# Performance work log

Hardware: AMD Instinct MI355X
Metric: run time of the kernel (lower is better)

Reference implementation:

```python
import jax, jax.numpy as jnp
import numpy as np

B, T, DIM, FF, E, TOPK = 2, 2048, 1024, 4096, 8, 2


def setup_inputs() -> dict:
    key = jax.random.key(0)
    k0, k1, k2, k3 = jax.random.split(key, 4)
    x = jax.random.normal(k0, (B, T, DIM), jnp.float32)
    # router weight [E, D] (nn.Linear(dim, num_experts, bias=False))
    Wr = jax.random.normal(k1, (E, DIM), jnp.float32) * (DIM ** -0.5)
    # per-expert FFN weights, stacked: W1 [E, D, FF], W2 [E, FF, D]
    W1 = jax.random.normal(k2, (E, DIM, FF), jnp.float32) * (DIM ** -0.5)
    W2 = jax.random.normal(k3, (E, FF, DIM), jnp.float32) * (FF ** -0.5)
    return {"x": x, "Wr": Wr, "W1": W1, "W2": W2}


def reference(x, Wr, W1, W2):
    """MoEFeedForward.forward, world_size=1, STANDARD implementation.

    Math: per token, top_k experts by router logits, softmax over the top_k
    logits (fp32), y = sum_k w_k * FFN_{e_k}(x). The torch code realizes this
    via sort/permute + per-expert variable-size GEMM + weighted index_add;
    the scatter-add result is identical to the dense masked form below,
    which is the jit-friendly (static-shape) expression.
    """
    Bn, Tn, D = x.shape
    num_experts = Wr.shape[0]
    xf = x.reshape(-1, D)                      # [N, D], N = B*T
    N = xf.shape[0]

    logits = xf @ Wr.T                         # [N, E]
    topw, topi = jax.lax.top_k(logits, TOPK)   # [N, K]
    topw = jax.nn.softmax(topw.astype(jnp.float32), axis=-1).astype(x.dtype)

    # combine weight for each (token, expert): [N, E] (0 if not routed)
    combine = jnp.zeros((N, num_experts), x.dtype)
    combine = combine.at[jnp.arange(N)[:, None], topi].add(topw)

    out = jnp.zeros_like(xf)
    for e in range(num_experts):               # fixed small loop over experts
        h = jax.nn.gelu(xf @ W1[e], approximate=False)  # exact GELU (nn.GELU)
        out = out + combine[:, e:e + 1] * (h @ W2[e])
    return out.reshape(Bn, Tn, D)
```

## Files before the change

kernel.cpp:

```cpp
#include <hip/hip_runtime.h>
#include <hip/hip_bf16.h>
#include <hip/hip_fp16.h>

#define NTOK 4096
#define DIM 1024
#define FF 4096
#define NE 8
#define NSLOT 8192

typedef _Float16 half8 __attribute__((ext_vector_type(8)));
typedef _Float16 half4 __attribute__((ext_vector_type(4)));
typedef float floatx4 __attribute__((ext_vector_type(4)));

__device__ __forceinline__ float gelu_exact(float x) {
    return 0.5f * x * (1.0f + erff(x * 0.70710678118654752f));
}

__device__ __forceinline__ void gl_lds16(const void* g, void* l) {
    __builtin_amdgcn_global_load_lds(
        (const __attribute__((address_space(1))) void*)g,
        (__attribute__((address_space(3))) void*)l, 16, 0, 0);
}

__device__ __forceinline__ void transpose_tile128(const float* __restrict__ s,
                                                  _Float16* __restrict__ d,
                                                  int R, int C, int r0, int c0,
                                                  char* smem) {
    float (*t)[66] = (float (*)[66])smem;
    int tid = threadIdx.x;
    int rr = tid >> 4, cc = (tid & 15) * 4;
#pragma unroll
    for (int i = 0; i < 8; ++i) {
        float4 v = *(const float4*)(s + (size_t)(r0 + rr + i * 16) * C + c0 + cc);
        t[rr + i * 16][cc] = v.x; t[rr + i * 16][cc + 1] = v.y;
        t[rr + i * 16][cc + 2] = v.z; t[rr + i * 16][cc + 3] = v.w;
    }
    __syncthreads();
#pragma unroll
    for (int j = 0; j < 4; ++j) {
        int chunk = j * 256 + tid;
        int fr = chunk >> 4, ch = chunk & 15;
        half8 v;
#pragma unroll
        for (int u = 0; u < 8; ++u) v[u] = (_Float16)t[ch * 8 + u][fr];
        *(half8*)(d + (size_t)(c0 + fr) * R + r0 + ch * 8) = v;
    }
}

__global__ __launch_bounds__(256) void k_prep(
    const float* __restrict__ x,
    const float* __restrict__ Wr,
    const float* __restrict__ W1,
    _Float16* __restrict__ w1t,
    _Float16* __restrict__ xh,
    int* __restrict__ counts,
    int* __restrict__ tok_e,
    float* __restrict__ tok_w,
    int* __restrict__ tok_pos) {
    __shared__ char smem[33792];
    int bid = blockIdx.x;
    int q = bid / 7, r = bid % 7;
    int tid = threadIdx.x;
    if (r < 4) {
        int t = q * 4 + r;
        int e = t >> 9, rem = t & 511;
        int r0 = (rem >> 6) << 7, c0 = (rem & 63) << 6;
        transpose_tile128(W1 + (size_t)e * DIM * FF, w1t + (size_t)e * FF * DIM,
                          DIM, FF, r0, c0, smem);
    } else if (r < 6) {
        int i = (q * 2 + (r - 4)) * 2048 + tid * 8;
        float4 a = *(const float4*)(x + i);
        float4 b = *(const float4*)(x + i + 4);
        half8 h;
        h[0] = (_Float16)a.x; h[1] = (_Float16)a.y; h[2] = (_Float16)a.z; h[3] = (_Float16)a.w;
        h[4] = (_Float16)b.x; h[5] = (_Float16)b.y; h[6] = (_Float16)b.z; h[7] = (_Float16)b.w;
        *(half8*)(xh + i) = h;
    } else {
        float* wr = (float*)smem;
        for (int i = tid; i < NE * DIM / 4; i += 256)
            ((float4*)wr)[i] = ((const float4*)Wr)[i];
        __syncthreads();
        int w = tid >> 6, lane = tid & 63;
        int t = q * 4 + w;
        float acc[NE] = {};
        for (int j = 0; j < DIM / 64; ++j) {
            float xv = x[t * DIM + j * 64 + lane];
#pragma unroll
            for (int e = 0; e < NE; ++e)
                acc[e] += xv * wr[e * DIM + j * 64 + lane];
        }
#pragma unroll
        for (int e = 0; e < NE; ++e) {
#pragma unroll
            for (int s = 32; s; s >>= 1) acc[e] += __shfl_xor(acc[e], s, 64);
        }
        if (lane == 0) {
            int b0 = 0; float m0 = acc[0];
#pragma unroll
            for (int e = 1; e < NE; ++e) { if (acc[e] > m0) { m0 = acc[e]; b0 = e; } }
            int b1 = -1; float m1 = -1e30f;
#pragma unroll
            for (int e = 0; e < NE; ++e) { if (e != b0 && acc[e] > m1) { m1 = acc[e]; b1 = e; } }
            float z = __expf(m1 - m0);
            float zz = 1.0f / (1.0f + z);
            int p0 = atomicAdd(&counts[b0], 1);
            int p1 = atomicAdd(&counts[b1], 1);
            tok_e[2 * t] = b0;  tok_e[2 * t + 1] = b1;
            tok_w[2 * t] = zz;  tok_w[2 * t + 1] = z * zz;
            tok_pos[2 * t] = p0; tok_pos[2 * t + 1] = p1;
        }
    }
}

__global__ __launch_bounds__(256) void k_transpose(const float* __restrict__ src,
                                                   _Float16* __restrict__ dst,
                                                   int R, int C) {
    __shared__ float t[64][65];
    int e = blockIdx.z;
    const float* s = src + (size_t)e * R * C;
    _Float16* d = dst + (size_t)e * C * R;
    int r0 = blockIdx.y * 64, c0 = blockIdx.x * 64;
    int tid = threadIdx.x;
    int rr = tid >> 4, cc = (tid & 15) * 4;
#pragma unroll
    for (int i = 0; i < 4; ++i) {
        float4 v = *(const float4*)(s + (size_t)(r0 + rr + i * 16) * C + c0 + cc);
        t[rr + i * 16][cc] = v.x; t[rr + i * 16][cc + 1] = v.y;
        t[rr + i * 16][cc + 2] = v.z; t[rr + i * 16][cc + 3] = v.w;
    }
    __syncthreads();
    int f = tid >> 3, ch = tid & 7;
#pragma unroll
    for (int j = 0; j < 2; ++j) {
        int fr = f + j * 32;
        half8 v;
#pragma unroll
        for (int u = 0; u < 8; ++u) v[u] = (_Float16)t[ch * 8 + u][fr];
        *(half8*)(d + (size_t)(c0 + fr) * R + r0 + ch * 8) = v;
    }
}

__global__ __launch_bounds__(256) void k_prefix_slots(
    const int* __restrict__ counts, int* __restrict__ offs,
    int* __restrict__ tmap256, int* __restrict__ tmap128,
    const int* __restrict__ tok_e, const int* __restrict__ tok_pos,
    int* __restrict__ tok_slot, int* __restrict__ list_tok) {
    __shared__ int soffs[NE];
    if (threadIdx.x == 0) {
        int s = 0, n2 = 0, n1 = 0;
        for (int e = 0; e < NE; ++e) {
            offs[e] = s; soffs[e] = s;
            int c = counts[e];
            for (int mt = 0; mt * 256 < c; ++mt) tmap256[1 + n2++] = (e << 16) | mt;
            for (int mt = 0; mt * 128 < c; ++mt) tmap128[1 + n1++] = (e << 16) | mt;
            s += c;
        }
        offs[NE] = s;
        tmap256[0] = n2;
        tmap128[0] = n1;
    }
    __syncthreads();
    for (int idx = threadIdx.x; idx < NSLOT; idx += 256) {
        int e = tok_e[idx];
        int slot = soffs[e] + tok_pos[idx];
        tok_slot[idx] = slot;
        list_tok[slot] = idx >> 1;
    }
}

template<int K, int NOUT, bool GATHER, bool GELU>
__device__ __forceinline__ void ffn128_body(
    const _Float16* __restrict__ Abase,
    const _Float16* __restrict__ Wbase,
    const int* __restrict__ counts,
    const int* __restrict__ offs,
    const int* __restrict__ list_tok,
    _Float16* __restrict__ Out,
    int e, int mt, int f0, _Float16* lds) {

    int base = offs[e] + mt * 128;
    int valid = counts[e] - mt * 128;

    int tid = threadIdx.x;
    int wid = tid >> 6, lane = tid & 63;

    const char* AB = (const char*)Abase;
    const char* WB = (const char*)(Wbase + (size_t)e * NOUT * K);

    size_t aoff[4]; unsigned boff[4];
#pragma unroll
    for (int i = 0; i < 4; ++i) {
        int g = wid * 256 + i * 64 + lane;
        int r = g >> 3;
        int c = (g & 7) ^ (r & 7);
        int rr = (r < valid) ? r : (valid - 1);
        unsigned arow = GATHER ? (unsigned)list_tok[base + rr] : (unsigned)(base + rr);
        aoff[i] = (size_t)arow * (K * 2) + c * 16;
        boff[i] = (unsigned)(f0 + r) * (unsigned)(K * 2) + c * 16;
    }

    floatx4 acc[4][4];
#pragma unroll
    for (int m = 0; m < 4; ++m)
#pragma unroll
        for (int n = 0; n < 4; ++n) acc[m][n] = (floatx4){0.f, 0.f, 0.f, 0.f};

    int la = lane & 15, lb = lane >> 4;
    int wm = (wid >> 1) * 64, wn = (wid & 1) * 64;

#pragma unroll
    for (int i = 0; i < 4; ++i)
        gl_lds16(AB + aoff[i], lds + wid * 2048 + i * 512);
#pragma unroll
    for (int i = 0; i < 4; ++i)
        gl_lds16(WB + boff[i], lds + 16384 + wid * 2048 + i * 512);
    asm volatile("s_waitcnt vmcnt(0)" ::: "memory");
    __builtin_amdgcn_s_barrier();
    __builtin_amdgcn_sched_barrier(0);

    constexpr int NT = K / 64;
#pragma unroll 2
    for (int t = 0; t < NT; ++t) {
        int cur = t & 1;
        if (t + 1 < NT) {
            size_t kadv = (size_t)(t + 1) * 128;
            _Float16* Ad = lds + (cur ^ 1) * 8192;
            _Float16* Bd = lds + 16384 + (cur ^ 1) * 8192;
#pragma unroll
            for (int i = 0; i < 4; ++i)
                gl_lds16(AB + aoff[i] + kadv, Ad + wid * 2048 + i * 512);
#pragma unroll
            for (int i = 0; i < 4; ++i)
                gl_lds16(WB + boff[i] + kadv, Bd + wid * 2048 + i * 512);
        }
        const _Float16* Ac = lds + cur * 8192;
        const _Float16* Bc = lds + 16384 + cur * 8192;
#pragma unroll
        for (int kk = 0; kk < 2; ++kk) {
            half8 af[4], bf[4];
#pragma unroll
            for (int m = 0; m < 4; ++m) {
                int row = wm + m * 16 + la;
                int c = kk * 4 + lb;
                af[m] = *(const half8*)(Ac + row * 64 + ((c ^ (row & 7)) * 8));
            }
#pragma unroll
            for (int n = 0; n < 4; ++n) {
                int row = wn + n * 16 + la;
                int c = kk * 4 + lb;
                bf[n] = *(const half8*)(Bc + row * 64 + ((c ^ (row & 7)) * 8));
            }
#pragma unroll
            for (int m = 0; m < 4; ++m)
#pragma unroll
                for (int n = 0; n < 4; ++n)
                    acc[m][n] = __builtin_amdgcn_mfma_f32_16x16x32_f16(af[m], bf[n], acc[m][n], 0, 0, 0);
        }
        __builtin_amdgcn_sched_barrier(0);
        asm volatile("s_waitcnt vmcnt(0)" ::: "memory");
        __builtin_amdgcn_s_barrier();
        __builtin_amdgcn_sched_barrier(0);
    }

    _Float16* tw = lds + wid * 4096;
#pragma unroll
    for (int m = 0; m < 4; ++m)
#pragma unroll
        for (int n = 0; n < 4; ++n) {
            floatx4 v = acc[m][n];
#pragma unroll
            for (int i = 0; i < 4; ++i) {
                float fv = v[i];
                if (GELU) fv = gelu_exact(fv);
                tw[(m * 16 + lb * 4 + i) * 64 + n * 16 + la] = (_Float16)fv;
            }
        }
    asm volatile("s_waitcnt lgkmcnt(0)" ::: "memory");
    __builtin_amdgcn_sched_barrier(0);
#pragma unroll
    for (int i = 0; i < 8; ++i) {
        int gi = i * 64 + lane;
        int row = gi >> 3, c8 = gi & 7;
        half8 v = *(const half8*)(tw + gi * 8);
        int trow = wm + row;
        if (trow < valid)
            *(half8*)(Out + (size_t)(base + trow) * NOUT + f0 + wn + c8 * 8) = v;
    }
}

template<int K, int NOUT, bool GATHER, bool GELU>
__global__ __launch_bounds__(256) void k_ffn(
    const _Float16* __restrict__ Abase,
    const _Float16* __restrict__ Wbase,
    const int* __restrict__ tmap,
    const int* __restrict__ counts,
    const int* __restrict__ offs,
    const int* __restrict__ list_tok,
    _Float16* __restrict__ Out) {
    __shared__ _Float16 lds[32768];
    int nt_m = tmap[0];
    if ((int)blockIdx.x >= nt_m) return;
    int ent = tmap[1 + blockIdx.x];
    ffn128_body<K, NOUT, GATHER, GELU>(Abase, Wbase, counts, offs, list_tok, Out,
                                       ent >> 16, ent & 0xffff, blockIdx.y * 128, lds);
}

__global__ __launch_bounds__(256) void k_ffn1_fused(
    const _Float16* __restrict__ xh,
    const _Float16* __restrict__ w1t,
    const int* __restrict__ tmap,
    const int* __restrict__ counts,
    const int* __restrict__ offs,
    const int* __restrict__ list_tok,
    _Float16* __restrict__ hbuf,
    const float* __restrict__ W2,
    _Float16* __restrict__ w2t) {
    __shared__ _Float16 lds[32768];
    int bid = blockIdx.x;
    int q = bid / 10, r = bid % 10;
    if (r < 2) {
        int f = q * 2 + r;
        int nt_m = tmap[0];
        int tile = f >> 5;
        if (tile >= nt_m) return;
        int ent = tmap[1 + tile];
        ffn128_body<DIM, FF, true, true>(xh, w1t, counts, offs, list_tok, hbuf,
                                         ent >> 16, ent & 0xffff, (f & 31) * 128, lds);
    } else {
        int t = q * 8 + (r - 2);
        if (t >= 8 * 32 * 16) return;
        int e = t >> 9, rem = t & 511;
        int r0 = (rem >> 4) << 7, c0 = (rem & 15) << 6;
        transpose_tile128(W2 + (size_t)e * FF * DIM, w2t + (size_t)e * DIM * FF,
                          FF, DIM, r0, c0, (char*)lds);
    }
}

template<int K, int NOUT, int KSPAN, bool GATHER, bool GELU>
__global__ __launch_bounds__(512, 2) void k_ffn256(
    const _Float16* __restrict__ Abase,
    const _Float16* __restrict__ Wbase,
    const int* __restrict__ tmap,
    const int* __restrict__ counts,
    const int* __restrict__ offs,
    const int* __restrict__ list_tok,
    _Float16* __restrict__ Out) {

    int nt_m = tmap[0];
    if ((int)blockIdx.x >= nt_m) return;
    int ent = tmap[1 + blockIdx.x];
    int e = ent >> 16, mt = ent & 0xffff;
    int base = offs[e] + mt * 256;
    int valid = counts[e] - mt * 256;
    int f0 = blockIdx.y * 256;
    int kbase = blockIdx.z * KSPAN;
    Out += (size_t)blockIdx.z * ((size_t)NSLOT * NOUT);

    __shared__ _Float16 lds[65536];

    int tid = threadIdx.x;
    int wid = tid >> 6, lane = tid & 63;

    const char* AB = (const char*)Abase;
    const char* WB = (const char*)(Wbase + (size_t)e * NOUT * K);

    size_t aoff[4]; unsigned boff[4];
#pragma unroll
    for (int i = 0; i < 4; ++i) {
        int g = i * 512 + tid;
        int r = g >> 3;
        int c = (g & 7) ^ (r & 7);
        int rr = (r < valid) ? r : (valid - 1);
        unsigned arow = GATHER ? (unsigned)list_tok[base + rr] : (unsigned)(base + rr);
        aoff[i] = (size_t)arow * (K * 2) + c * 16 + (size_t)kbase * 2;
        boff[i] = (unsigned)(f0 + r) * (unsigned)(K * 2) + c * 16 + (unsigned)kbase * 2;
    }

    floatx4 acc[8][4];
#pragma unroll
    for (int m = 0; m < 8; ++m)
#pragma unroll
        for (int n = 0; n < 4; ++n) acc[m][n] = (floatx4){0.f, 0.f, 0.f, 0.f};

    int la = lane & 15, lb = lane >> 4;
    int wmb = (wid >> 2) * 128, wnb = (wid & 3) * 64;

#pragma unroll
    for (int i = 0; i < 4; ++i)
        gl_lds16(AB + aoff[i], lds + i * 4096 + wid * 512);
#pragma unroll
    for (int i = 0; i < 4; ++i)
        gl_lds16(WB + boff[i], lds + 32768 + i * 4096 + wid * 512);
    asm volatile("s_waitcnt vmcnt(0)" ::: "memory");
    __builtin_amdgcn_s_barrier();
    __builtin_amdgcn_sched_barrier(0);

    constexpr int NT = KSPAN / 64;
#pragma unroll 2
    for (int t = 0; t < NT; ++t) {
        int cur = t & 1;
        if (t + 1 < NT) {
            size_t adv = (size_t)(t + 1) * 128;
            _Float16* Ad = lds + (cur ^ 1) * 16384;
            _Float16* Bd = lds + 32768 + (cur ^ 1) * 16384;
#pragma unroll
            for (int i = 0; i < 4; ++i)
                gl_lds16(AB + aoff[i] + adv, Ad + i * 4096 + wid * 512);
#pragma unroll
            for (int i = 0; i < 4; ++i)
                gl_lds16(WB + boff[i] + adv, Bd + i * 4096 + wid * 512);
        }
        const _Float16* Ac = lds + cur * 16384;
        const _Float16* Bc = lds + 32768 + cur * 16384;
#pragma unroll
        for (int kk = 0; kk < 2; ++kk) {
            half8 af[8], bf[4];
#pragma unroll
            for (int n = 0; n < 4; ++n) {
                int row = wnb + n * 16 + la;
                int c = kk * 4 + lb;
                bf[n] = *(const half8*)(Bc + row * 64 + ((c ^ (row & 7)) * 8));
            }
#pragma unroll
            for (int m = 0; m < 8; ++m) {
                int row = wmb + m * 16 + la;
                int c = kk * 4 + lb;
                af[m] = *(const half8*)(Ac + row * 64 + ((c ^ (row & 7)) * 8));
            }
#pragma unroll
            for (int m = 0; m < 8; ++m)
#pragma unroll
                for (int n = 0; n < 4; ++n)
                    acc[m][n] = __builtin_amdgcn_mfma_f32_16x16x32_f16(af[m], bf[n], acc[m][n], 0, 0, 0);
        }
        __builtin_amdgcn_sched_barrier(0);
        asm volatile("s_waitcnt vmcnt(0)" ::: "memory");
        __builtin_amdgcn_s_barrier();
        __builtin_amdgcn_sched_barrier(0);
    }

    _Float16* tw = lds + wid * 4096;
#pragma unroll
    for (int ps = 0; ps < 2; ++ps) {
#pragma unroll
        for (int fi = 0; fi < 4; ++fi)
#pragma unroll
            for (int nf = 0; nf < 4; ++nf) {
                floatx4 v = acc[ps * 4 + fi][nf];
#pragma unroll
                for (int i2 = 0; i2 < 4; ++i2) {
                    float fv = v[i2];
                    if (GELU) fv = gelu_exact(fv);
                    tw[(fi * 16 + lb * 4 + i2) * 64 + nf * 16 + la] = (_Float16)fv;
                }
            }
        asm volatile("s_waitcnt lgkmcnt(0)" ::: "memory");
        __builtin_amdgcn_sched_barrier(0);
#pragma unroll
        for (int i2 = 0; i2 < 8; ++i2) {
            int gi = i2 * 64 + lane;
            int row = gi >> 3, c8 = gi & 7;
            half8 v = *(const half8*)(tw + gi * 8);
            int trow = wmb + ps * 64 + row;
            if (trow < valid)
                *(half8*)(Out + (size_t)(base + trow) * NOUT + f0 + wnb + c8 * 8) = v;
        }
    }
}

__global__ __launch_bounds__(256) void k_combine(const _Float16* __restrict__ yp,
                                                 const int* __restrict__ tok_slot,
                                                 const float* __restrict__ tok_w,
                                                 float* __restrict__ out,
                                                 int nsplit) {
    int t = blockIdx.x;
    int d = threadIdx.x * 4;
    int s0 = tok_slot[2 * t], s1 = tok_slot[2 * t + 1];
    float w0 = tok_w[2 * t], w1 = tok_w[2 * t + 1];
    float4 sum0 = {0.f, 0.f, 0.f, 0.f}, sum1 = {0.f, 0.f, 0.f, 0.f};
    for (int z = 0; z < nsplit; ++z) {
        const _Float16* p = yp + (size_t)z * NSLOT * DIM;
        half4 y0 = *(const half4*)(p + (size_t)s0 * DIM + d);
        half4 y1 = *(const half4*)(p + (size_t)s1 * DIM + d);
        sum0.x += (float)y0[0]; sum0.y += (float)y0[1];
        sum0.z += (float)y0[2]; sum0.w += (float)y0[3];
        sum1.x += (float)y1[0]; sum1.y += (float)y1[1];
        sum1.z += (float)y1[2]; sum1.w += (float)y1[3];
    }
    float4 o;
    o.x = w0 * sum0.x + w1 * sum1.x;
    o.y = w0 * sum0.y + w1 * sum1.y;
    o.z = w0 * sum0.z + w1 * sum1.z;
    o.w = w0 * sum0.w + w1 * sum1.w;
    *(float4*)(out + (size_t)t * DIM + d) = o;
}

extern "C" void kernel_launch(void* const* d_in, const int* in_sizes, int n_in,
                              void* d_out, int out_size, void* d_ws, size_t ws_size,
                              hipStream_t stream) {
    const float* x  = (const float*)d_in[0];
    const float* Wr = (const float*)d_in[1];
    const float* W1 = (const float*)d_in[2];
    const float* W2 = (const float*)d_in[3];
    float* out = (float*)d_out;

    char* ws = (char*)d_ws;
    _Float16* w1t  = (_Float16*)ws;
    _Float16* xh   = (_Float16*)(ws + 67108864);
    _Float16* hbuf = (_Float16*)(ws + 75497472);
    char* p = ws + 142606336;
    int*   counts   = (int*)p;        p += 1024;
    int*   offs     = (int*)p;        p += 1024;
    int*   tmap256  = (int*)p;        p += 1024;
    int*   tmap128  = (int*)p;        p += 1024;
    int*   tok_e    = (int*)p;        p += NSLOT * 4;
    float* tok_w    = (float*)p;      p += NSLOT * 4;
    int*   tok_pos  = (int*)p;        p += NSLOT * 4;
    int*   tok_slot = (int*)p;        p += NSLOT * 4;
    int*   list_tok = (int*)p;        p += NSLOT * 4;
    const size_t OFF_EXT = 142606336 + 196608;
    const size_t SZ_Y  = (size_t)NSLOT * DIM * 2;
    const size_t SZ_WT = (size_t)NE * DIM * FF * 2;

    bool fused = (ws_size >= OFF_EXT + SZ_WT);

    hipMemsetAsync(counts, 0, NE * sizeof(int), stream);
    k_prep<<<7 * 1024, 256, 0, stream>>>(x, Wr, W1, w1t, xh,
                                         counts, tok_e, tok_w, tok_pos);
    k_prefix_slots<<<1, 256, 0, stream>>>(counts, offs, tmap256, tmap128,
                                          tok_e, tok_pos, tok_slot, list_tok);

    if (fused) {
        _Float16* w2t = (_Float16*)(ws + OFF_EXT);
        _Float16* yp  = (_Float16*)ws;
        k_ffn1_fused<<<10 * 1152, 256, 0, stream>>>(
            xh, w1t, tmap128, counts, offs, list_tok, hbuf, W2, w2t);
        k_ffn256<FF, DIM, 1024, false, false>
            <<<dim3(NSLOT / 256 + NE, DIM / 256, 4), 512, 0, stream>>>(
                hbuf, w2t, tmap256, counts, offs, list_tok, yp);
        k_combine<<<NTOK, 256, 0, stream>>>(yp, tok_slot, tok_w, out, 4);
    } else {
        _Float16* w2t = w1t;
        _Float16* yp  = (_Float16*)(ws + OFF_EXT);
        int nsplit = (ws_size >= OFF_EXT + 2 * SZ_Y) ? 2 : 1;
        k_ffn<DIM, FF, true, true>
            <<<dim3(NSLOT / 128 + NE, FF / 128), 256, 0, stream>>>(
                xh, w1t, tmap128, counts, offs, list_tok, hbuf);
        k_transpose<<<dim3(DIM / 64, FF / 64, NE), 256, 0, stream>>>(W2, w2t, FF, DIM);
        if (nsplit == 2) {
            k_ffn256<FF, DIM, 2048, false, false>
                <<<dim3(NSLOT / 256 + NE, DIM / 256, 2), 512, 0, stream>>>(
                    hbuf, w2t, tmap256, counts, offs, list_tok, yp);
        } else {
            k_ffn<FF, DIM, false, false>
                <<<dim3(NSLOT / 128 + NE, DIM / 128), 256, 0, stream>>>(
                    hbuf, w2t, tmap128, counts, offs, list_tok, yp);
        }
        k_combine<<<NTOK, 256, 0, stream>>>(yp, tok_slot, tok_w, out, nsplit);
    }
}
```

Baseline: 372.6 us.

## Fold prefix-slot kernel into prep via completion counter and swizzle transpose LDS

Removes the separate single-block prefix/slot kernel launch. An extra last block of the prep kernel spin-waits on an atomic counter of finished router blocks, then computes offsets, tile maps and slot lists. This relies on that block being scheduled after the others and only hides launch gap. Separately, the W1 transpose tile uses an XOR-swizzled unpadded LDS layout with float4 stores instead of a padded array with scalar stores, to cut bank conflicts.

```diff
diff --git a/kernel.cpp b/kernel.cpp
--- a/kernel.cpp
+++ b/kernel.cpp
@@ -26,14 +26,14 @@
                                                   _Float16* __restrict__ d,
                                                   int R, int C, int r0, int c0,
                                                   char* smem) {
-    float (*t)[66] = (float (*)[66])smem;
+    float* t = (float*)smem;
     int tid = threadIdx.x;
     int rr = tid >> 4, cc = (tid & 15) * 4;
 #pragma unroll
     for (int i = 0; i < 8; ++i) {
-        float4 v = *(const float4*)(s + (size_t)(r0 + rr + i * 16) * C + c0 + cc);
-        t[rr + i * 16][cc] = v.x; t[rr + i * 16][cc + 1] = v.y;
-        t[rr + i * 16][cc + 2] = v.z; t[rr + i * 16][cc + 3] = v.w;
+        int r = rr + i * 16;
+        float4 v = *(const float4*)(s + (size_t)(r0 + r) * C + c0 + cc);
+        *(float4*)(t + r * 64 + (cc ^ (((r >> 3) & 15) << 2))) = v;
     }
     __syncthreads();
 #pragma unroll
@@ -42,7 +42,8 @@
         int fr = chunk >> 4, ch = chunk & 15;
         half8 v;
 #pragma unroll
-        for (int u = 0; u < 8; ++u) v[u] = (_Float16)t[ch * 8 + u][fr];
+        for (int u = 0; u < 8; ++u)
+            v[u] = (_Float16)t[(ch * 8 + u) * 64 + (fr ^ (ch << 2))];
         *(half8*)(d + (size_t)(c0 + fr) * R + r0 + ch * 8) = v;
     }
 }
@@ -54,13 +55,51 @@
     _Float16* __restrict__ w1t,
     _Float16* __restrict__ xh,
     int* __restrict__ counts,
+    int* __restrict__ offs,
+    int* __restrict__ tmap256,
+    int* __restrict__ tmap128,
     int* __restrict__ tok_e,
     float* __restrict__ tok_w,
-    int* __restrict__ tok_pos) {
-    __shared__ char smem[33792];
+    int* __restrict__ tok_pos,
+    int* __restrict__ tok_slot,
+    int* __restrict__ list_tok) {
+    __shared__ char smem[32768];
     int bid = blockIdx.x;
+    int tid = threadIdx.x;
+    int* rdone = counts + 8;
+
+    if (bid == 7168) {
+        if (tid == 0) {
+            while (__hip_atomic_load(rdone, __ATOMIC_ACQUIRE, __HIP_MEMORY_SCOPE_AGENT) < 1024)
+                __builtin_amdgcn_s_sleep(8);
+        }
+        __syncthreads();
+        (void)__hip_atomic_load(rdone, __ATOMIC_ACQUIRE, __HIP_MEMORY_SCOPE_AGENT);
+        int* soffs = (int*)smem;
+        if (tid == 0) {
+            int s = 0, n2 = 0, n1 = 0;
+            for (int e = 0; e < NE; ++e) {
+                offs[e] = s; soffs[e] = s;
+                int c = counts[e];
+                for (int mt = 0; mt * 256 < c; ++mt) tmap256[1 + n2++] = (e << 16) | mt;
+                for (int mt = 0; mt * 128 < c; ++mt) tmap128[1 + n1++] = (e << 16) | mt;
+                s += c;
+            }
+            offs[NE] = s;
+            tmap256[0] = n2;
+            tmap128[0] = n1;
+        }
+        __syncthreads();
+        for (int idx = tid; idx < NSLOT; idx += 256) {
+            int e = tok_e[idx];
+            int slot = soffs[e] + tok_pos[idx];
+            tok_slot[idx] = slot;
+            list_tok[slot] = idx >> 1;
+        }
+        return;
+    }
+
     int q = bid / 7, r = bid % 7;
-    int tid = threadIdx.x;
     if (r < 4) {
         int t = q * 4 + r;
         int e = t >> 9, rem = t & 511;
@@ -108,7 +147,11 @@
             tok_e[2 * t] = b0;  tok_e[2 * t + 1] = b1;
             tok_w[2 * t] = zz;  tok_w[2 * t + 1] = z * zz;
             tok_pos[2 * t] = p0; tok_pos[2 * t + 1] = p1;
-        }
+            __threadfence();
+        }
+        __syncthreads();
+        if (tid == 0)
+            __hip_atomic_fetch_add(rdone, 1, __ATOMIC_RELEASE, __HIP_MEMORY_SCOPE_AGENT);
     }
 }
 
@@ -137,34 +180,6 @@
 #pragma unroll
         for (int u = 0; u < 8; ++u) v[u] = (_Float16)t[ch * 8 + u][fr];
         *(half8*)(d + (size_t)(c0 + fr) * R + r0 + ch * 8) = v;
-    }
-}
-
-__global__ __launch_bounds__(256) void k_prefix_slots(
-    const int* __restrict__ counts, int* __restrict__ offs,
-    int* __restrict__ tmap256, int* __restrict__ tmap128,
-    const int* __restrict__ tok_e, const int* __restrict__ tok_pos,
-    int* __restrict__ tok_slot, int* __restrict__ list_tok) {
-    __shared__ int soffs[NE];
-    if (threadIdx.x == 0) {
-        int s = 0, n2 = 0, n1 = 0;
-        for (int e = 0; e < NE; ++e) {
-            offs[e] = s; soffs[e] = s;
-            int c = counts[e];
-            for (int mt = 0; mt * 256 < c; ++mt) tmap256[1 + n2++] = (e << 16) | mt;
-            for (int mt = 0; mt * 128 < c; ++mt) tmap128[1 + n1++] = (e << 16) | mt;
-            s += c;
-        }
-        offs[NE] = s;
-        tmap256[0] = n2;
-        tmap128[0] = n1;
-    }
-    __syncthreads();
-    for (int idx = threadIdx.x; idx < NSLOT; idx += 256) {
-        int e = tok_e[idx];
-        int slot = soffs[e] + tok_pos[idx];
-        tok_slot[idx] = slot;
-        list_tok[slot] = idx >> 1;
     }
 }
 
@@ -524,11 +539,10 @@
 
     bool fused = (ws_size >= OFF_EXT + SZ_WT);
 
-    hipMemsetAsync(counts, 0, NE * sizeof(int), stream);
-    k_prep<<<7 * 1024, 256, 0, stream>>>(x, Wr, W1, w1t, xh,
-                                         counts, tok_e, tok_w, tok_pos);
-    k_prefix_slots<<<1, 256, 0, stream>>>(counts, offs, tmap256, tmap128,
-                                          tok_e, tok_pos, tok_slot, list_tok);
+    hipMemsetAsync(counts, 0, 64, stream);
+    k_prep<<<7 * 1024 + 1, 256, 0, stream>>>(x, Wr, W1, w1t, xh,
+                                             counts, offs, tmap256, tmap128,
+                                             tok_e, tok_w, tok_pos, tok_slot, list_tok);
 
     if (fused) {
         _Float16* w2t = (_Float16*)(ws + OFF_EXT);
```

Result: slower. 529.8 us (+42.2%).
